# Kernel optimization log

Hardware: AMD Instinct MI355X
Metric: run time of the kernel (lower is better)

## Reference

```python
import jax, jax.numpy as jnp
import numpy as np

DIM = 512
HIDDEN = 1024
H2 = HIDDEN // 2
B = 384


def setup_inputs() -> dict:
    key = jax.random.key(0)
    ks = jax.random.split(key, 10)
    s_in = 1.0 / np.sqrt(DIM)
    s_h = 1.0 / np.sqrt(H2)
    return {
        "x_samples": jax.random.normal(ks[0], (B, DIM), dtype=jnp.float32),
        "y_samples": jax.random.normal(ks[1], (B, DIM), dtype=jnp.float32),
        "w1_mu": jax.random.uniform(ks[2], (DIM, H2), jnp.float32, -s_in, s_in),
        "b1_mu": jax.random.uniform(ks[3], (H2,), jnp.float32, -s_in, s_in),
        "w2_mu": jax.random.uniform(ks[4], (H2, DIM), jnp.float32, -s_h, s_h),
        "b2_mu": jax.random.uniform(ks[5], (DIM,), jnp.float32, -s_h, s_h),
        "w1_lv": jax.random.uniform(ks[6], (DIM, H2), jnp.float32, -s_in, s_in),
        "b1_lv": jax.random.uniform(ks[7], (H2,), jnp.float32, -s_in, s_in),
        "w2_lv": jax.random.uniform(ks[8], (H2, DIM), jnp.float32, -s_h, s_h),
        "b2_lv": jax.random.uniform(ks[9], (DIM,), jnp.float32, -s_h, s_h),
    }


def reference(x_samples, y_samples, w1_mu, b1_mu, w2_mu, b2_mu,
              w1_lv, b1_lv, w2_lv, b2_lv):
    batch_size = y_samples.shape[0]
    # p_mu / p_logvar MLPs
    mu = jax.nn.relu(x_samples @ w1_mu + b1_mu) @ w2_mu + b2_mu           # [B, D]
    logvar = jnp.tanh(jax.nn.relu(x_samples @ w1_lv + b1_lv) @ w2_lv + b2_lv)  # [B, D]
    inv_var = jnp.exp(-logvar)

    # positive log-likelihood per sample
    positive = (-(mu - y_samples) ** 2 * 0.5 * inv_var - logvar * 0.5).sum(-1)  # [B]

    # pairwise Gaussian log-likelihoods: all_probs[i, j] = log N(y_j; mu_i)
    diff = y_samples[None, :, :] - mu[:, None, :]                          # [B, B, D]
    all_probs = (-diff ** 2 * 0.5 * inv_var[:, None, :]
                 - logvar[:, None, :] * 0.5).sum(-1)                       # [B, B]

    # faithful to the torch broadcast: [B,B] + [B,B,1] -> [B,B,B]
    diag_mask = jnp.eye(batch_size, dtype=jnp.float32)[:, :, None] * -20.0  # [B, B, 1]
    scores = all_probs + diag_mask                                         # [B, B, B]
    negative = jax.scipy.special.logsumexp(scores, axis=0) - jnp.log(batch_size - 1.0)  # [B, B]

    upper = (positive - negative).mean()

    loglikeli = (-(mu - y_samples) ** 2 * inv_var - logvar).sum(1).mean(0)
    return loglikeli + jax.lax.stop_gradient(-loglikeli + upper)
```

## Files before the change

### kernel.cpp

```cpp
#include <hip/hip_runtime.h>
#include <math.h>

#define NROW 384
#define NCOL 512

#define HP_OFF   0
#define GP_OFF   786432
#define M1_OFF   1572864
#define M2_OFF   1575936
#define PART_OFF 1579008
#define CNT_OFF  1579392

template<bool COMBINE>
__device__ __forceinline__ void gemm32x64(
    const float* __restrict__ A0, const float* __restrict__ A1,
    const float* __restrict__ bias1,
    const float* __restrict__ W, float* __restrict__ C,
    int m0, int n0, int ca)
{
    __shared__ __align__(16) float As[32][34];
    __shared__ __align__(16) float Bs[32][64];

    const int t  = threadIdx.x;
    const int tx = t & 15;
    const int ty = t >> 4;
    const int r_a = t >> 3;
    const int kg  = (t & 7) * 4;
    const int kr  = t >> 4;
    const int cg  = (t & 15) * 4;

    float4 a_pf0, a_pf1, c_pf0, c_pf1, bb_pf;
    float4 b_pf[4];

    auto load_iter = [&](int k0) {
        const float* a0p = &A0[(size_t)(m0 + r_a) * NCOL + ca + k0 + kg];
        a_pf0 = *(const float4*)a0p;
        a_pf1 = *(const float4*)(a0p + 16 * NCOL);
        if (COMBINE) {
            const float* a1p = &A1[(size_t)(m0 + r_a) * NCOL + ca + k0 + kg];
            c_pf0 = *(const float4*)a1p;
            c_pf1 = *(const float4*)(a1p + 16 * NCOL);
            bb_pf = *(const float4*)&bias1[ca + k0 + kg];
        }
        #pragma unroll
        for (int i = 0; i < 4; ++i)
            b_pf[i] = *(const float4*)&W[(size_t)(ca + k0 + kr + 8 * i) * NCOL + n0 + cg];
    };

    float acc[4][4] = {};
    load_iter(0);

    for (int it = 0; it < 8; ++it) {
        __syncthreads();
        {
            float av0[4], av1[4];
            *(float4*)av0 = a_pf0; *(float4*)av1 = a_pf1;
            if (COMBINE) {
                float cv0[4], cv1[4], bv[4];
                *(float4*)cv0 = c_pf0; *(float4*)cv1 = c_pf1;
                *(float4*)bv  = bb_pf;
                #pragma unroll
                for (int j = 0; j < 4; ++j) {
                    av0[j] = fmaxf(av0[j] + cv0[j] + bv[j], 0.f);
                    av1[j] = fmaxf(av1[j] + cv1[j] + bv[j], 0.f);
                }
            }
            #pragma unroll
            for (int j = 0; j < 4; ++j) {
                As[kg + j][r_a]      = av0[j];
                As[kg + j][r_a + 16] = av1[j];
            }
            #pragma unroll
            for (int i = 0; i < 4; ++i)
                *(float4*)&Bs[kr + 8 * i][cg] = b_pf[i];
        }
        __syncthreads();
        if (it < 7) load_iter((it + 1) * 32);

        #pragma unroll
        for (int kk = 0; kk < 32; ++kk) {
            float av[4], bv[4];
            *(float2*)&av[0] = *(const float2*)&As[kk][ty * 4];
            *(float2*)&av[2] = *(const float2*)&As[kk][ty * 4 + 2];
            *(float4*)bv     = *(const float4*)&Bs[kk][tx * 4];
            #pragma unroll
            for (int i = 0; i < 4; ++i) {
                acc[i][0] += av[i] * bv[0];
                acc[i][1] += av[i] * bv[1];
                acc[i][2] += av[i] * bv[2];
                acc[i][3] += av[i] * bv[3];
            }
        }
    }

    #pragma unroll
    for (int i = 0; i < 4; ++i) {
        float4 o = make_float4(acc[i][0], acc[i][1], acc[i][2], acc[i][3]);
        *(float4*)&C[(size_t)(m0 + ty * 4 + i) * NCOL + n0 + tx * 4] = o;
    }
}

__global__ __launch_bounds__(128, 2) void k_layer1(
    const float* __restrict__ x,
    const float* __restrict__ w1mu, const float* __restrict__ w1lv,
    const float* __restrict__ y, float* __restrict__ ws)
{
    const int b = blockIdx.x;
    const int t = threadIdx.x;

    if (b == 0 && t == 0) *(int*)(ws + CNT_OFF) = 0;

    if (b >= 384) {
        const int sb = b - 384;
        const int c  = t * 4;
        float s1[4] = {0.f, 0.f, 0.f, 0.f};
        float s2[4] = {0.f, 0.f, 0.f, 0.f};
        #pragma unroll 4
        for (int r = 0; r < 64; ++r) {
            float v[4];
            *(float4*)v = *(const float4*)&y[(size_t)(sb * 64 + r) * NCOL + c];
            #pragma unroll
            for (int j = 0; j < 4; ++j) { s1[j] += v[j]; s2[j] += v[j] * v[j]; }
        }
        *(float4*)&ws[M1_OFF + sb * NCOL + c] = make_float4(s1[0], s1[1], s1[2], s1[3]);
        *(float4*)&ws[M2_OFF + sb * NCOL + c] = make_float4(s2[0], s2[1], s2[2], s2[3]);
        return;
    }

    const int branch = b / 192;
    const int rem    = b % 192;
    const int sl     = rem / 96;
    const int mt     = (rem % 96) >> 3;
    const int nt     = rem & 7;

    const float* W = branch ? w1lv : w1mu;
    float* C = ws + HP_OFF + (size_t)(branch * 2 + sl) * 196608;
    gemm32x64<false>(x, nullptr, nullptr, W, C, mt * 32, nt * 64, sl * 256);
}

__global__ __launch_bounds__(128, 2) void k_layer2(
    const float* __restrict__ w2mu, const float* __restrict__ b1mu,
    const float* __restrict__ w2lv, const float* __restrict__ b1lv,
    float* __restrict__ ws)
{
    const int b = blockIdx.x;
    const int branch = b / 192;
    const int rem    = b % 192;
    const int sl     = rem / 96;
    const int mt     = (rem % 96) >> 3;
    const int nt     = rem & 7;

    const float* A0 = ws + HP_OFF + (size_t)(branch * 2 + 0) * 196608;
    const float* A1 = ws + HP_OFF + (size_t)(branch * 2 + 1) * 196608;
    const float* bias1 = branch ? b1lv : b1mu;
    const float* W = branch ? w2lv : w2mu;
    float* C = ws + GP_OFF + (size_t)(branch * 2 + sl) * 196608;
    gemm32x64<true>(A0, A1, bias1, W, C, mt * 32, nt * 64, sl * 256);
}

__global__ __launch_bounds__(256) void k_epilogue(
    const float* __restrict__ b2mu, const float* __restrict__ b2lv,
    const float* __restrict__ y, float* __restrict__ ws,
    float* __restrict__ out)
{
    __shared__ double wsum[4];
    __shared__ int is_last;

    const int t = threadIdx.x;
    const float inv_b = 1.0f / (float)NROW;

    const int e4   = blockIdx.x * 256 + t;
    const int col4 = e4 & 127;
    const size_t off = (size_t)e4 * 4;

    const float* gm0 = ws + GP_OFF;
    const float* gm1 = ws + GP_OFF + 196608;
    const float* gl0 = ws + GP_OFF + 2 * 196608;
    const float* gl1 = ws + GP_OFF + 3 * 196608;

    float gm[4], gq[4], gl[4], gr[4], yv[4], bm[4], bl[4], s1[4], s2[4];
    *(float4*)gm = *(const float4*)&gm0[off];
    *(float4*)gq = *(const float4*)&gm1[off];
    *(float4*)gl = *(const float4*)&gl0[off];
    *(float4*)gr = *(const float4*)&gl1[off];
    *(float4*)yv = *(const float4*)&y[off];
    *(float4*)bm = *(const float4*)&b2mu[col4 * 4];
    *(float4*)bl = *(const float4*)&b2lv[col4 * 4];
    #pragma unroll
    for (int j = 0; j < 4; ++j) { s1[j] = 0.f; s2[j] = 0.f; }
    #pragma unroll
    for (int p = 0; p < 6; ++p) {
        float p1[4], p2[4];
        *(float4*)p1 = *(const float4*)&ws[M1_OFF + p * NCOL + col4 * 4];
        *(float4*)p2 = *(const float4*)&ws[M2_OFF + p * NCOL + col4 * 4];
        #pragma unroll
        for (int j = 0; j < 4; ++j) { s1[j] += p1[j]; s2[j] += p2[j]; }
    }

    float tsum = 0.f;
    #pragma unroll
    for (int j = 0; j < 4; ++j) {
        const float m1 = s1[j] * inv_b;
        const float m2 = s2[j] * inv_b;
        const float mu = gm[j] + gq[j] + bm[j];
        const float lv = tanhf(gl[j] + gr[j] + bl[j]);
        const float iv = expf(-lv);
        tsum += iv * ((yv[j] * yv[j] - m2) + 2.f * mu * (m1 - yv[j]));
    }

    float s = tsum;
    #pragma unroll
    for (int o = 32; o > 0; o >>= 1) s += __shfl_down(s, o);
    if ((t & 63) == 0) wsum[t >> 6] = (double)s;
    __syncthreads();

    double* partials = (double*)(ws + PART_OFF);
    int* counter = (int*)(ws + CNT_OFF);
    if (t == 0) {
        partials[blockIdx.x] = wsum[0] + wsum[1] + wsum[2] + wsum[3];
        __threadfence();
        const int old = atomicAdd(counter, 1);
        is_last = (old == 191) ? 1 : 0;
    }
    __syncthreads();

    if (is_last && t < 64) {
        __threadfence();
        double v = partials[t] + partials[t + 64] + partials[t + 128];
        #pragma unroll
        for (int o = 32; o > 0; o >>= 1) v += __shfl_down(v, o);
        if (t == 0) {
            const double C0 = 5.381602146862063e-12;
            out[0] = (float)(-0.5 * v / (double)NROW - C0);
        }
    }
}

extern "C" void kernel_launch(void* const* d_in, const int* in_sizes, int n_in,
                              void* d_out, int out_size, void* d_ws, size_t ws_size,
                              hipStream_t stream) {
    const float* x    = (const float*)d_in[0];
    const float* y    = (const float*)d_in[1];
    const float* w1mu = (const float*)d_in[2];
    const float* b1mu = (const float*)d_in[3];
    const float* w2mu = (const float*)d_in[4];
    const float* b2mu = (const float*)d_in[5];
    const float* w1lv = (const float*)d_in[6];
    const float* b1lv = (const float*)d_in[7];
    const float* w2lv = (const float*)d_in[8];
    const float* b2lv = (const float*)d_in[9];
    float* out = (float*)d_out;
    float* ws  = (float*)d_ws;

    k_layer1<<<390, 128, 0, stream>>>(x, w1mu, w1lv, y, ws);
    k_layer2<<<384, 128, 0, stream>>>(w2mu, b1mu, w2lv, b1lv, ws);
    k_epilogue<<<192, 256, 0, stream>>>(b2mu, b2lv, y, ws, out);
}
```

Measured before the change: 118.5 us.

## Split-K four ways with double-buffered LDS and move mean-reduction into layer2

Doubles the split-K factor from 2 to 4 in both GEMM layers, so each kernel launches twice as many blocks (768 instead of 384), each doing half the K work. The shared-memory tiles become double-buffered with padding, which drops one barrier per iteration and allows float4 LDS reads of A. The y column sums are now split over 12 partial blocks and reduced by an extra block in layer2 instead of in every epilogue block. The aim is better CU occupancy on a small problem, paid for with more partial-sum traffic through the workspace (4 slices per branch) and more reads in the epilogue.

```diff
diff --git a/kernel.cpp b/kernel.cpp
--- a/kernel.cpp
+++ b/kernel.cpp
@@ -5,84 +5,92 @@
 #define NCOL 512
 
 #define HP_OFF   0
-#define GP_OFF   786432
-#define M1_OFF   1572864
-#define M2_OFF   1575936
-#define PART_OFF 1579008
-#define CNT_OFF  1579392
-
-template<bool COMBINE>
-__device__ __forceinline__ void gemm32x64(
-    const float* __restrict__ A0, const float* __restrict__ A1,
-    const float* __restrict__ bias1,
+#define GP_OFF   1572864
+#define M1P_OFF  3145728
+#define M2P_OFF  3151872
+#define M1_OFF   3158016
+#define M2_OFF   3158528
+#define PART_OFF 3159040
+#define CNT_OFF  3159424
+#define SLICE    196608
+
+template<int NS>
+__device__ __forceinline__ void gemm_block(
+    const float* __restrict__ A, const float* __restrict__ bias1,
     const float* __restrict__ W, float* __restrict__ C,
     int m0, int n0, int ca)
 {
-    __shared__ __align__(16) float As[32][34];
-    __shared__ __align__(16) float Bs[32][64];
+    __shared__ __align__(16) float As[2][32][36];
+    __shared__ __align__(16) float Bs[2][32][68];
 
     const int t  = threadIdx.x;
     const int tx = t & 15;
     const int ty = t >> 4;
-    const int r_a = t >> 3;
-    const int kg  = (t & 7) * 4;
-    const int kr  = t >> 4;
-    const int cg  = (t & 15) * 4;
-
-    float4 a_pf0, a_pf1, c_pf0, c_pf1, bb_pf;
-    float4 b_pf[4];
-
-    auto load_iter = [&](int k0) {
-        const float* a0p = &A0[(size_t)(m0 + r_a) * NCOL + ca + k0 + kg];
-        a_pf0 = *(const float4*)a0p;
-        a_pf1 = *(const float4*)(a0p + 16 * NCOL);
-        if (COMBINE) {
-            const float* a1p = &A1[(size_t)(m0 + r_a) * NCOL + ca + k0 + kg];
-            c_pf0 = *(const float4*)a1p;
-            c_pf1 = *(const float4*)(a1p + 16 * NCOL);
-            bb_pf = *(const float4*)&bias1[ca + k0 + kg];
-        }
-        #pragma unroll
-        for (int i = 0; i < 4; ++i)
-            b_pf[i] = *(const float4*)&W[(size_t)(ca + k0 + kr + 8 * i) * NCOL + n0 + cg];
+    const int am0 = t >> 3;
+    const int ak4 = (t & 7) * 4;
+    const int bk  = t >> 4;
+    const int bn4 = (t & 15) * 4;
+
+    float4 a_raw[2][NS];
+    float4 b_raw[4];
+    float4 bias_raw;
+
+    auto load_it = [&](int k0) {
+        #pragma unroll
+        for (int p = 0; p < 2; ++p) {
+            const size_t aoff = (size_t)(m0 + am0 + p * 16) * NCOL + ca + k0 + ak4;
+            #pragma unroll
+            for (int s = 0; s < NS; ++s)
+                a_raw[p][s] = *(const float4*)&A[(size_t)s * SLICE + aoff];
+        }
+        if (NS > 1) bias_raw = *(const float4*)&bias1[ca + k0 + ak4];
+        #pragma unroll
+        for (int q = 0; q < 4; ++q)
+            b_raw[q] = *(const float4*)&W[(size_t)(ca + k0 + bk + 8 * q) * NCOL + n0 + bn4];
     };
 
+    auto store_it = [&](int buf) {
+        #pragma unroll
+        for (int p = 0; p < 2; ++p) {
+            float v[4];
+            if (NS == 1) {
+                *(float4*)v = a_raw[p][0];
+            } else {
+                float s0[4], s1[4], s2[4], s3[4], bb[4];
+                *(float4*)s0 = a_raw[p][0]; *(float4*)s1 = a_raw[p][1];
+                *(float4*)s2 = a_raw[p][2]; *(float4*)s3 = a_raw[p][3];
+                *(float4*)bb = bias_raw;
+                #pragma unroll
+                for (int j = 0; j < 4; ++j)
+                    v[j] = fmaxf(s0[j] + s1[j] + s2[j] + s3[j] + bb[j], 0.f);
+            }
+            #pragma unroll
+            for (int j = 0; j < 4; ++j)
+                As[buf][ak4 + j][am0 + p * 16] = v[j];
+        }
+        #pragma unroll
+        for (int q = 0; q < 4; ++q)
+            *(float4*)&Bs[buf][bk + 8 * q][bn4] = b_raw[q];
+    };
+
     float acc[4][4] = {};
-    load_iter(0);
-
-    for (int it = 0; it < 8; ++it) {
-        __syncthreads();
-        {
-            float av0[4], av1[4];
-            *(float4*)av0 = a_pf0; *(float4*)av1 = a_pf1;
-            if (COMBINE) {
-                float cv0[4], cv1[4], bv[4];
-                *(float4*)cv0 = c_pf0; *(float4*)cv1 = c_pf1;
-                *(float4*)bv  = bb_pf;
-                #pragma unroll
-                for (int j = 0; j < 4; ++j) {
-                    av0[j] = fmaxf(av0[j] + cv0[j] + bv[j], 0.f);
-                    av1[j] = fmaxf(av1[j] + cv1[j] + bv[j], 0.f);
-                }
-            }
-            #pragma unroll
-            for (int j = 0; j < 4; ++j) {
-                As[kg + j][r_a]      = av0[j];
-                As[kg + j][r_a + 16] = av1[j];
-            }
-            #pragma unroll
-            for (int i = 0; i < 4; ++i)
-                *(float4*)&Bs[kr + 8 * i][cg] = b_pf[i];
-        }
-        __syncthreads();
-        if (it < 7) load_iter((it + 1) * 32);
-
+
+    load_it(0);
+    store_it(0);
+    __syncthreads();
+    load_it(32);
+
+    for (int it = 0; it < 4; ++it) {
+        if (it < 3) {
+            store_it((it + 1) & 1);
+            if (it < 2) load_it((it + 2) * 32);
+        }
+        const int buf = it & 1;
         #pragma unroll
         for (int kk = 0; kk < 32; ++kk) {
             float av[4], bv[4];
-            *(float2*)&av[0] = *(const float2*)&As[kk][ty * 4];
-            *(float2*)&av[2] = *(const float2*)&As[kk][ty * 4 + 2];
-            *(float4*)bv     = *(const float4*)&Bs[kk][tx * 4];
+            *(float4*)av = *(const float4*)&As[buf][kk][ty * 4];
+            *(float4*)bv = *(const float4*)&Bs[buf][kk][tx * 4];
             #pragma unroll
             for (int i = 0; i < 4; ++i) {
                 acc[i][0] += av[i] * bv[0];
@@ -91,13 +99,13 @@
                 acc[i][3] += av[i] * bv[3];
             }
         }
-    }
-
-    #pragma unroll
-    for (int i = 0; i < 4; ++i) {
-        float4 o = make_float4(acc[i][0], acc[i][1], acc[i][2], acc[i][3]);
-        *(float4*)&C[(size_t)(m0 + ty * 4 + i) * NCOL + n0 + tx * 4] = o;
-    }
+        __syncthreads();
+    }
+
+    #pragma unroll
+    for (int i = 0; i < 4; ++i)
+        *(float4*)&C[(size_t)(m0 + ty * 4 + i) * NCOL + n0 + tx * 4] =
+            make_float4(acc[i][0], acc[i][1], acc[i][2], acc[i][3]);
 }
 
 __global__ __launch_bounds__(128, 2) void k_layer1(
@@ -108,54 +116,70 @@
     const int b = blockIdx.x;
     const int t = threadIdx.x;
 
-    if (b == 0 && t == 0) *(int*)(ws + CNT_OFF) = 0;
-
-    if (b >= 384) {
-        const int sb = b - 384;
+    if (b >= 768) {
+        const int sb = b - 768;
         const int c  = t * 4;
         float s1[4] = {0.f, 0.f, 0.f, 0.f};
         float s2[4] = {0.f, 0.f, 0.f, 0.f};
         #pragma unroll 4
-        for (int r = 0; r < 64; ++r) {
+        for (int r = 0; r < 32; ++r) {
             float v[4];
-            *(float4*)v = *(const float4*)&y[(size_t)(sb * 64 + r) * NCOL + c];
+            *(float4*)v = *(const float4*)&y[(size_t)(sb * 32 + r) * NCOL + c];
             #pragma unroll
             for (int j = 0; j < 4; ++j) { s1[j] += v[j]; s2[j] += v[j] * v[j]; }
         }
-        *(float4*)&ws[M1_OFF + sb * NCOL + c] = make_float4(s1[0], s1[1], s1[2], s1[3]);
-        *(float4*)&ws[M2_OFF + sb * NCOL + c] = make_float4(s2[0], s2[1], s2[2], s2[3]);
+        *(float4*)&ws[M1P_OFF + sb * NCOL + c] = make_float4(s1[0], s1[1], s1[2], s1[3]);
+        *(float4*)&ws[M2P_OFF + sb * NCOL + c] = make_float4(s2[0], s2[1], s2[2], s2[3]);
         return;
     }
 
-    const int branch = b / 192;
-    const int rem    = b % 192;
-    const int sl     = rem / 96;
-    const int mt     = (rem % 96) >> 3;
-    const int nt     = rem & 7;
-
-    const float* W = branch ? w1lv : w1mu;
-    float* C = ws + HP_OFF + (size_t)(branch * 2 + sl) * 196608;
-    gemm32x64<false>(x, nullptr, nullptr, W, C, mt * 32, nt * 64, sl * 256);
+    const int sl   = b & 3;
+    const int br   = (b >> 2) & 1;
+    const int tile = b >> 3;
+    const int mt   = tile >> 3;
+    const int nt   = tile & 7;
+
+    gemm_block<1>(x, nullptr, br ? w1lv : w1mu,
+                  ws + HP_OFF + (size_t)(br * 4 + sl) * SLICE,
+                  mt * 32, nt * 64, sl * 128);
 }
 
 __global__ __launch_bounds__(128, 2) void k_layer2(
-    const float* __restrict__ w2mu, const float* __restrict__ b1mu,
-    const float* __restrict__ w2lv, const float* __restrict__ b1lv,
+    const float* __restrict__ b1mu, const float* __restrict__ b1lv,
+    const float* __restrict__ w2mu, const float* __restrict__ w2lv,
     float* __restrict__ ws)
 {
     const int b = blockIdx.x;
-    const int branch = b / 192;
-    const int rem    = b % 192;
-    const int sl     = rem / 96;
-    const int mt     = (rem % 96) >> 3;
-    const int nt     = rem & 7;
-
-    const float* A0 = ws + HP_OFF + (size_t)(branch * 2 + 0) * 196608;
-    const float* A1 = ws + HP_OFF + (size_t)(branch * 2 + 1) * 196608;
-    const float* bias1 = branch ? b1lv : b1mu;
-    const float* W = branch ? w2lv : w2mu;
-    float* C = ws + GP_OFF + (size_t)(branch * 2 + sl) * 196608;
-    gemm32x64<true>(A0, A1, bias1, W, C, mt * 32, nt * 64, sl * 256);
+    const int t = threadIdx.x;
+
+    if (b == 768) {
+        if (t == 0) *(int*)(ws + CNT_OFF) = 0;
+        const int c = t * 4;
+        float s1[4] = {0.f, 0.f, 0.f, 0.f};
+        float s2[4] = {0.f, 0.f, 0.f, 0.f};
+        #pragma unroll
+        for (int p = 0; p < 12; ++p) {
+            float p1[4], p2[4];
+            *(float4*)p1 = *(const float4*)&ws[M1P_OFF + p * NCOL + c];
+            *(float4*)p2 = *(const float4*)&ws[M2P_OFF + p * NCOL + c];
+            #pragma unroll
+            for (int j = 0; j < 4; ++j) { s1[j] += p1[j]; s2[j] += p2[j]; }
+        }
+        *(float4*)&ws[M1_OFF + c] = make_float4(s1[0], s1[1], s1[2], s1[3]);
+        *(float4*)&ws[M2_OFF + c] = make_float4(s2[0], s2[1], s2[2], s2[3]);
+        return;
+    }
+
+    const int sl   = b & 3;
+    const int br   = (b >> 2) & 1;
+    const int tile = b >> 3;
+    const int mt   = tile >> 3;
+    const int nt   = tile & 7;
+
+    gemm_block<4>(ws + HP_OFF + (size_t)(br * 4) * SLICE,
+                  br ? b1lv : b1mu, br ? w2lv : w2mu,
+                  ws + GP_OFF + (size_t)(br * 4 + sl) * SLICE,
+                  mt * 32, nt * 64, sl * 128);
 }
 
 __global__ __launch_bounds__(256) void k_epilogue(
@@ -173,37 +197,34 @@
     const int col4 = e4 & 127;
     const size_t off = (size_t)e4 * 4;
 
-    const float* gm0 = ws + GP_OFF;
-    const float* gm1 = ws + GP_OFF + 196608;
-    const float* gl0 = ws + GP_OFF + 2 * 196608;
-    const float* gl1 = ws + GP_OFF + 3 * 196608;
-
-    float gm[4], gq[4], gl[4], gr[4], yv[4], bm[4], bl[4], s1[4], s2[4];
-    *(float4*)gm = *(const float4*)&gm0[off];
-    *(float4*)gq = *(const float4*)&gm1[off];
-    *(float4*)gl = *(const float4*)&gl0[off];
-    *(float4*)gr = *(const float4*)&gl1[off];
-    *(float4*)yv = *(const float4*)&y[off];
-    *(float4*)bm = *(const float4*)&b2mu[col4 * 4];
-    *(float4*)bl = *(const float4*)&b2lv[col4 * 4];
-    #pragma unroll
-    for (int j = 0; j < 4; ++j) { s1[j] = 0.f; s2[j] = 0.f; }
-    #pragma unroll
-    for (int p = 0; p < 6; ++p) {
-        float p1[4], p2[4];
-        *(float4*)p1 = *(const float4*)&ws[M1_OFF + p * NCOL + col4 * 4];
-        *(float4*)p2 = *(const float4*)&ws[M2_OFF + p * NCOL + col4 * 4];
-        #pragma unroll
-        for (int j = 0; j < 4; ++j) { s1[j] += p1[j]; s2[j] += p2[j]; }
-    }
+    const float* gpm = ws + GP_OFF;
+    const float* gpl = ws + GP_OFF + 4 * SLICE;
+
+    float gm[4] = {0.f, 0.f, 0.f, 0.f};
+    float gl[4] = {0.f, 0.f, 0.f, 0.f};
+    #pragma unroll
+    for (int s = 0; s < 4; ++s) {
+        float a[4], c[4];
+        *(float4*)a = *(const float4*)&gpm[(size_t)s * SLICE + off];
+        *(float4*)c = *(const float4*)&gpl[(size_t)s * SLICE + off];
+        #pragma unroll
+        for (int j = 0; j < 4; ++j) { gm[j] += a[j]; gl[j] += c[j]; }
+    }
+
+    float yv[4], bm[4], bl[4], m1v[4], m2v[4];
+    *(float4*)yv  = *(const float4*)&y[off];
+    *(float4*)bm  = *(const float4*)&b2mu[col4 * 4];
+    *(float4*)bl  = *(const float4*)&b2lv[col4 * 4];
+    *(float4*)m1v = *(const float4*)&ws[M1_OFF + col4 * 4];
+    *(float4*)m2v = *(const float4*)&ws[M2_OFF + col4 * 4];
 
     float tsum = 0.f;
     #pragma unroll
     for (int j = 0; j < 4; ++j) {
-        const float m1 = s1[j] * inv_b;
-        const float m2 = s2[j] * inv_b;
-        const float mu = gm[j] + gq[j] + bm[j];
-        const float lv = tanhf(gl[j] + gr[j] + bl[j]);
+        const float m1 = m1v[j] * inv_b;
+        const float m2 = m2v[j] * inv_b;
+        const float mu = gm[j] + bm[j];
+        const float lv = tanhf(gl[j] + bl[j]);
         const float iv = expf(-lv);
         tsum += iv * ((yv[j] * yv[j] - m2) + 2.f * mu * (m1 - yv[j]));
     }
@@ -252,7 +273,7 @@
     float* out = (float*)d_out;
     float* ws  = (float*)d_ws;
 
-    k_layer1<<<390, 128, 0, stream>>>(x, w1mu, w1lv, y, ws);
-    k_layer2<<<384, 128, 0, stream>>>(w2mu, b1mu, w2lv, b1lv, ws);
+    k_layer1<<<780, 128, 0, stream>>>(x, w1mu, w1lv, y, ws);
+    k_layer2<<<769, 128, 0, stream>>>(b1mu, b1lv, w2mu, w2lv, ws);
     k_epilogue<<<192, 256, 0, stream>>>(b2mu, b2lv, y, ws, out);
 }
```

Result: faster. 112.2 us (-5.4%).
